# Kernel tuning notes

Measured on AMD Instinct MI355X. Metric: run time of the kernel, lower is better.

The kernel has to match this reference:

```python
import jax, jax.numpy as jnp
import numpy as np

OUT_SIZE = 224  # hardcoded in the torch forward: F.interpolate(size=224)


def _lin_interp_axis(x, axis, out_size):
    """1D linear interpolation along `axis` with align_corners=True."""
    in_size = x.shape[axis]
    # align_corners=True: src = dst * (in-1)/(out-1)
    pos = jnp.arange(out_size, dtype=jnp.float32) * ((in_size - 1) / (out_size - 1))
    i0 = jnp.clip(jnp.floor(pos).astype(jnp.int32), 0, in_size - 2)
    w = pos - i0.astype(jnp.float32)
    x0 = jnp.take(x, i0, axis=axis)
    x1 = jnp.take(x, i0 + 1, axis=axis)
    bshape = [1] * x.ndim
    bshape[axis] = out_size
    w = w.reshape(bshape)
    return x0 * (1.0 - w) + x1 * w


def setup_inputs() -> dict:
    key = jax.random.key(0)
    k1, k2, k3 = jax.random.split(key, 3)
    hidden, n_classes = 32, 4
    x = jax.random.normal(k1, (1, hidden, 14, 14, 14), dtype=jnp.float32)
    # 1x1x1 conv3d == per-voxel channel matmul; store kernel as [out, in]
    W = jax.random.normal(k2, (n_classes, hidden), dtype=jnp.float32) / np.sqrt(hidden)
    b = jax.random.normal(k3, (n_classes,), dtype=jnp.float32) * 0.01
    return {"x": x, "W": W, "b": b}


def reference(x, W, b):
    # Trilinear upsample (separable linear interp per spatial axis),
    # upsampling smallest dims first keeps peak memory low.
    y = _lin_interp_axis(x, 2, OUT_SIZE)   # [B,C,224,14,14]
    y = _lin_interp_axis(y, 3, OUT_SIZE)   # [B,C,224,224,14]
    y = _lin_interp_axis(y, 4, OUT_SIZE)   # [B,C,224,224,224]
    # 1x1x1 conv3d: per-voxel channel contraction
    z = jnp.einsum('bcdhw,oc->bodhw', y, W) + b[None, :, None, None, None]
    # softmax over channel dim (dim=1)
    return jax.nn.softmax(z, axis=1)
```

## Files before the change

kernel.cpp:

```cpp
#include <hip/hip_runtime.h>
#include <hip/hip_bf16.h>


#define NSP 2744
#define NV  11239424
#define RATIO (13.0f / 223.0f)

__global__ __launch_bounds__(256) void conv_small(
    const float* __restrict__ x,
    const float* __restrict__ W,
    const float* __restrict__ b,
    float4* __restrict__ z)
{
    int s = blockIdx.x * 256 + threadIdx.x;
    if (s >= NSP) return;
    float a0 = b[0], a1 = b[1], a2 = b[2], a3 = b[3];
#pragma unroll
    for (int c = 0; c < 32; ++c) {
        float xv = x[c * NSP + s];
        a0 = fmaf(W[c],      xv, a0);
        a1 = fmaf(W[32 + c], xv, a1);
        a2 = fmaf(W[64 + c], xv, a2);
        a3 = fmaf(W[96 + c], xv, a3);
    }
    z[s] = make_float4(a0, a1, a2, a3);
}

__device__ __forceinline__ float4 bilerp4(const float4* __restrict__ zs,
                                          int b00, int b01, int b10, int b11,
                                          int iw,
                                          float c00, float c01, float c10, float c11)
{
    float4 A = zs[b00 + iw], B = zs[b01 + iw], C = zs[b10 + iw], D = zs[b11 + iw];
    float4 r;
    r.x = fmaf(c11, D.x, fmaf(c10, C.x, fmaf(c01, B.x, c00 * A.x)));
    r.y = fmaf(c11, D.y, fmaf(c10, C.y, fmaf(c01, B.y, c00 * A.y)));
    r.z = fmaf(c11, D.z, fmaf(c10, C.z, fmaf(c01, B.z, c00 * A.z)));
    r.w = fmaf(c11, D.w, fmaf(c10, C.w, fmaf(c01, B.w, c00 * A.w)));
    return r;
}

__global__ __launch_bounds__(512) void upsample_softmax(
    const float4* __restrict__ z,
    float* __restrict__ out)
{
    __shared__ float4 zs[NSP];
    for (int k = threadIdx.x; k < NSP; k += 512) zs[k] = z[k];
    __syncthreads();

    unsigned gid = blockIdx.x * 512u + threadIdx.x;
    unsigned w4  = gid % 56u;
    unsigned row = gid / 56u;
    unsigned hh  = row % 224u;
    unsigned dd  = row / 224u;

    float posd = (float)dd * RATIO;
    int   i0d  = min((int)posd, 12);
    float wd   = posd - (float)i0d;
    float posh = (float)hh * RATIO;
    int   i0h  = min((int)posh, 12);
    float wh   = posh - (float)i0h;

    int   wb    = (int)w4 * 4;
    float posw0 = (float)wb * RATIO;
    int   iw0   = min((int)posw0, 12);

    float c11 = wd * wh;
    float c10 = wd - c11;
    float c01 = wh - c11;
    float c00 = 1.0f - wd - wh + c11;

    int b00 = (i0d * 14 + i0h) * 14;
    int b01 = b00 + 14;
    int b10 = b00 + 196;
    int b11 = b00 + 210;

    float4 g0 = bilerp4(zs, b00, b01, b10, b11, iw0,              c00, c01, c10, c11);
    float4 g1 = bilerp4(zs, b00, b01, b10, b11, iw0 + 1,          c00, c01, c10, c11);
    float4 g2 = bilerp4(zs, b00, b01, b10, b11, min(iw0 + 2, 13), c00, c01, c10, c11);

    float4 d10, d21;
    d10.x = g1.x - g0.x; d10.y = g1.y - g0.y; d10.z = g1.z - g0.z; d10.w = g1.w - g0.w;
    d21.x = g2.x - g1.x; d21.y = g2.y - g1.y; d21.z = g2.z - g1.z; d21.w = g2.w - g1.w;

    const float LOG2E = 1.44269504088896340736f;
    float4 res[4];
#pragma unroll
    for (int j = 0; j < 4; ++j) {
        float posw = (float)(wb + j) * RATIO;
        int   i0w  = min((int)posw, 12);
        float ww   = posw - (float)i0w;
        bool  hi   = (i0w > iw0);
        float bx = hi ? g1.x : g0.x, by = hi ? g1.y : g0.y,
              bz = hi ? g1.z : g0.z, bw = hi ? g1.w : g0.w;
        float ex = hi ? d21.x : d10.x, ey = hi ? d21.y : d10.y,
              ez = hi ? d21.z : d10.z, ew = hi ? d21.w : d10.w;
        float v0 = fmaf(ww, ex, bx);
        float v1 = fmaf(ww, ey, by);
        float v2 = fmaf(ww, ez, bz);
        float v3 = fmaf(ww, ew, bw);
        float t0 = v0 * LOG2E, t1 = v1 * LOG2E, t2 = v2 * LOG2E, t3 = v3 * LOG2E;
        float m  = fmaxf(fmaxf(t0, t1), fmaxf(t2, t3));
        float e0 = exp2f(t0 - m), e1 = exp2f(t1 - m), e2 = exp2f(t2 - m), e3 = exp2f(t3 - m);
        float s  = (e0 + e1) + (e2 + e3);
        float inv = __builtin_amdgcn_rcpf(s);
        res[j].x = e0 * inv;
        res[j].y = e1 * inv;
        res[j].z = e2 * inv;
        res[j].w = e3 * inv;
    }

    unsigned sidx = row * 224u + (unsigned)wb;
    float4 o0 = make_float4(res[0].x, res[1].x, res[2].x, res[3].x);
    float4 o1 = make_float4(res[0].y, res[1].y, res[2].y, res[3].y);
    float4 o2 = make_float4(res[0].z, res[1].z, res[2].z, res[3].z);
    float4 o3 = make_float4(res[0].w, res[1].w, res[2].w, res[3].w);
    *(float4*)(out + 0u * NV + sidx) = o0;
    *(float4*)(out + 1u * NV + sidx) = o1;
    *(float4*)(out + 2u * NV + sidx) = o2;
    *(float4*)(out + 3u * NV + sidx) = o3;
}

extern "C" void kernel_launch(void* const* d_in, const int* in_sizes, int n_in,
                              void* d_out, int out_size, void* d_ws, size_t ws_size,
                              hipStream_t stream) {
    const float* x = (const float*)d_in[0];
    const float* W = (const float*)d_in[1];
    const float* b = (const float*)d_in[2];
    float* out = (float*)d_out;
    float4* z = (float4*)d_ws;

    conv_small<<<(NSP + 255) / 256, 256, 0, stream>>>(x, W, b, z);
    upsample_softmax<<<(NV / 4) / 512, 512, 0, stream>>>(z, out);
}
```

Baseline: 184.7 us.

## Compute 16 outputs per thread, drop LDS staging, prescale logits by log2e

Each thread now produces 16 consecutive w outputs instead of 4, computing the three bilinear samples once per segment. The shared-memory copy of the z table and its block barrier are removed; the table is read straight from global memory, where it should stay cache-resident. The LOG2E scaling moves into the conv kernel, and the softmax max-subtraction is dropped. The w interpolation now uses clamped piecewise weights instead of select logic. Without max-subtraction exp2 could overflow for large logits, and writing 16 values per thread changes the store pattern and occupancy.

Result: slower. 240.8 us (+30.3%).

```diff
diff --git a/kernel.cpp b/kernel.cpp
--- a/kernel.cpp
+++ b/kernel.cpp
@@ -3,8 +3,8 @@
 
 
 #define NSP 2744
-#define NV  11239424
-#define RATIO (13.0f / 223.0f)
+#define NV  11239424u
+#define RATIO 0.0582959641255605381166f
 
 __global__ __launch_bounds__(256) void conv_small(
     const float* __restrict__ x,
@@ -23,15 +23,15 @@
         a2 = fmaf(W[64 + c], xv, a2);
         a3 = fmaf(W[96 + c], xv, a3);
     }
-    z[s] = make_float4(a0, a1, a2, a3);
+    const float LOG2E = 1.44269504088896340736f;
+    z[s] = make_float4(a0 * LOG2E, a1 * LOG2E, a2 * LOG2E, a3 * LOG2E);
 }
 
-__device__ __forceinline__ float4 bilerp4(const float4* __restrict__ zs,
-                                          int b00, int b01, int b10, int b11,
-                                          int iw,
+__device__ __forceinline__ float4 bilerp4(const float4* __restrict__ z,
+                                          int b00, int iw,
                                           float c00, float c01, float c10, float c11)
 {
-    float4 A = zs[b00 + iw], B = zs[b01 + iw], C = zs[b10 + iw], D = zs[b11 + iw];
+    float4 A = z[b00 + iw], B = z[b00 + 14 + iw], C = z[b00 + 196 + iw], D = z[b00 + 210 + iw];
     float4 r;
     r.x = fmaf(c11, D.x, fmaf(c10, C.x, fmaf(c01, B.x, c00 * A.x)));
     r.y = fmaf(c11, D.y, fmaf(c10, C.y, fmaf(c01, B.y, c00 * A.y)));
@@ -40,17 +40,13 @@
     return r;
 }
 
-__global__ __launch_bounds__(512) void upsample_softmax(
+__global__ __launch_bounds__(256) void upsample_softmax(
     const float4* __restrict__ z,
     float* __restrict__ out)
 {
-    __shared__ float4 zs[NSP];
-    for (int k = threadIdx.x; k < NSP; k += 512) zs[k] = z[k];
-    __syncthreads();
-
-    unsigned gid = blockIdx.x * 512u + threadIdx.x;
-    unsigned w4  = gid % 56u;
-    unsigned row = gid / 56u;
+    unsigned gid = blockIdx.x * 256u + threadIdx.x;
+    unsigned seg = gid % 14u;
+    unsigned row = gid / 14u;
     unsigned hh  = row % 224u;
     unsigned dd  = row / 224u;
 
@@ -61,64 +57,52 @@
     int   i0h  = min((int)posh, 12);
     float wh   = posh - (float)i0h;
 
-    int   wb    = (int)w4 * 4;
-    float posw0 = (float)wb * RATIO;
-    int   iw0   = min((int)posw0, 12);
-
     float c11 = wd * wh;
     float c10 = wd - c11;
     float c01 = wh - c11;
     float c00 = 1.0f - wd - wh + c11;
+    int b00 = (i0d * 14 + i0h) * 14;
 
-    int b00 = (i0d * 14 + i0h) * 14;
-    int b01 = b00 + 14;
-    int b10 = b00 + 196;
-    int b11 = b00 + 210;
+    int   wb    = (int)seg * 16;
+    float posw0 = (float)wb * RATIO;
+    int   iw0   = min((int)posw0, 12);
+    float u0    = posw0 - (float)iw0;
 
-    float4 g0 = bilerp4(zs, b00, b01, b10, b11, iw0,              c00, c01, c10, c11);
-    float4 g1 = bilerp4(zs, b00, b01, b10, b11, iw0 + 1,          c00, c01, c10, c11);
-    float4 g2 = bilerp4(zs, b00, b01, b10, b11, min(iw0 + 2, 13), c00, c01, c10, c11);
+    float4 g0 = bilerp4(z, b00, iw0,              c00, c01, c10, c11);
+    float4 g1 = bilerp4(z, b00, iw0 + 1,          c00, c01, c10, c11);
+    float4 g2 = bilerp4(z, b00, min(iw0 + 2, 13), c00, c01, c10, c11);
 
     float4 d10, d21;
     d10.x = g1.x - g0.x; d10.y = g1.y - g0.y; d10.z = g1.z - g0.z; d10.w = g1.w - g0.w;
     d21.x = g2.x - g1.x; d21.y = g2.y - g1.y; d21.z = g2.z - g1.z; d21.w = g2.w - g1.w;
 
-    const float LOG2E = 1.44269504088896340736f;
-    float4 res[4];
+    unsigned sbase = row * 224u + (unsigned)wb;
 #pragma unroll
-    for (int j = 0; j < 4; ++j) {
-        float posw = (float)(wb + j) * RATIO;
-        int   i0w  = min((int)posw, 12);
-        float ww   = posw - (float)i0w;
-        bool  hi   = (i0w > iw0);
-        float bx = hi ? g1.x : g0.x, by = hi ? g1.y : g0.y,
-              bz = hi ? g1.z : g0.z, bw = hi ? g1.w : g0.w;
-        float ex = hi ? d21.x : d10.x, ey = hi ? d21.y : d10.y,
-              ez = hi ? d21.z : d10.z, ew = hi ? d21.w : d10.w;
-        float v0 = fmaf(ww, ex, bx);
-        float v1 = fmaf(ww, ey, by);
-        float v2 = fmaf(ww, ez, bz);
-        float v3 = fmaf(ww, ew, bw);
-        float t0 = v0 * LOG2E, t1 = v1 * LOG2E, t2 = v2 * LOG2E, t3 = v3 * LOG2E;
-        float m  = fmaxf(fmaxf(t0, t1), fmaxf(t2, t3));
-        float e0 = exp2f(t0 - m), e1 = exp2f(t1 - m), e2 = exp2f(t2 - m), e3 = exp2f(t3 - m);
-        float s  = (e0 + e1) + (e2 + e3);
-        float inv = __builtin_amdgcn_rcpf(s);
-        res[j].x = e0 * inv;
-        res[j].y = e1 * inv;
-        res[j].z = e2 * inv;
-        res[j].w = e3 * inv;
+    for (int q = 0; q < 4; ++q) {
+        float och[4][4];
+#pragma unroll
+        for (int jj = 0; jj < 4; ++jj) {
+            float u  = fmaf((float)(q * 4 + jj), RATIO, u0);
+            float u1 = fminf(u, 1.0f);
+            float u2 = fmaxf(u - 1.0f, 0.0f);
+            float t0 = fmaf(u2, d21.x, fmaf(u1, d10.x, g0.x));
+            float t1 = fmaf(u2, d21.y, fmaf(u1, d10.y, g0.y));
+            float t2 = fmaf(u2, d21.z, fmaf(u1, d10.z, g0.z));
+            float t3 = fmaf(u2, d21.w, fmaf(u1, d10.w, g0.w));
+            float e0 = exp2f(t0), e1 = exp2f(t1), e2 = exp2f(t2), e3 = exp2f(t3);
+            float s   = (e0 + e1) + (e2 + e3);
+            float inv = __builtin_amdgcn_rcpf(s);
+            och[0][jj] = e0 * inv;
+            och[1][jj] = e1 * inv;
+            och[2][jj] = e2 * inv;
+            och[3][jj] = e3 * inv;
+        }
+        unsigned sidx = sbase + (unsigned)(q * 4);
+        *(float4*)(out + 0u * NV + sidx) = make_float4(och[0][0], och[0][1], och[0][2], och[0][3]);
+        *(float4*)(out + 1u * NV + sidx) = make_float4(och[1][0], och[1][1], och[1][2], och[1][3]);
+        *(float4*)(out + 2u * NV + sidx) = make_float4(och[2][0], och[2][1], och[2][2], och[2][3]);
+        *(float4*)(out + 3u * NV + sidx) = make_float4(och[3][0], och[3][1], och[3][2], och[3][3]);
     }
-
-    unsigned sidx = row * 224u + (unsigned)wb;
-    float4 o0 = make_float4(res[0].x, res[1].x, res[2].x, res[3].x);
-    float4 o1 = make_float4(res[0].y, res[1].y, res[2].y, res[3].y);
-    float4 o2 = make_float4(res[0].z, res[1].z, res[2].z, res[3].z);
-    float4 o3 = make_float4(res[0].w, res[1].w, res[2].w, res[3].w);
-    *(float4*)(out + 0u * NV + sidx) = o0;
-    *(float4*)(out + 1u * NV + sidx) = o1;
-    *(float4*)(out + 2u * NV + sidx) = o2;
-    *(float4*)(out + 3u * NV + sidx) = o3;
 }
 
 extern "C" void kernel_launch(void* const* d_in, const int* in_sizes, int n_in,
@@ -131,5 +115,5 @@
     float4* z = (float4*)d_ws;
 
     conv_small<<<(NSP + 255) / 256, 256, 0, stream>>>(x, W, b, z);
-    upsample_softmax<<<(NV / 4) / 512, 512, 0, stream>>>(z, out);
+    upsample_softmax<<<702464u / 256u, 256, 0, stream>>>(z, out);
 }
```
